# Kernel tuning notes

Hardware: AMD Instinct MI355X
Metric: run time of the kernel (lower is better)

Reference implementation:

```python
import jax, jax.numpy as jnp
import numpy as np

H, DK = 16, 64
F = H * DK  # n_feat = 1024
B, T = 2, 2048


def setup_inputs() -> dict:
    key = jax.random.key(0)
    ks = jax.random.split(key, 11)
    mk = lambda k, sh: jax.random.normal(k, sh, dtype=jnp.float32)
    inp = {
        "query": mk(ks[0], (B, T, F)),
        "key": mk(ks[1], (B, T, F)),
        "value": mk(ks[2], (B, T, F)),
    }
    # Standard RoPE frequency table, shaped [T,1,1,DK] to broadcast over [t,b,h,d].
    pos = jnp.arange(T, dtype=jnp.float32)[:, None]
    inv_freq = 1.0 / (10000.0 ** (jnp.arange(0, DK, 2, dtype=jnp.float32) / DK))
    ang = pos * inv_freq                       # [T, DK/2]
    emb = jnp.concatenate([ang, ang], axis=-1)  # [T, DK]
    inp["cos"] = jnp.cos(emb)[:, None, None, :]
    inp["sin"] = jnp.sin(emb)[:, None, None, :]
    scale = 1.0 / np.sqrt(F).astype(np.float32)
    for i, n in enumerate(["wq", "wk", "wv", "wo"]):
        inp[n] = mk(ks[3 + i], (F, F)) * scale  # torch Linear weight layout [out,in]
    for i, n in enumerate(["bq", "bk", "bv", "bo"]):
        inp[n] = mk(ks[7 + i], (F,)) * 0.01
    return inp


def _rtt_half(x):
    d = x.shape[-1]
    return jnp.concatenate([-x[..., d // 2:], x[..., :d // 2]], axis=-1)


def reference(query, key, value, cos, sin, wq, bq, wk, bk, wv, bv, wo, bo):
    b, t, f = query.shape
    h, d = H, DK
    # [b,t,f] -> [t,b,h,d] as in the torch code (RoPE applied pre-projection)
    to_tbhd = lambda x: jnp.swapaxes(x, 0, 1).reshape(t, b, h, d)
    q = to_tbhd(query)
    k = to_tbhd(key)
    c, s = cos[:t], sin[:t]
    q = q * c + _rtt_half(q) * s
    k = k * c + _rtt_half(k) * s
    back = lambda x: jnp.swapaxes(x.reshape(t, b, f), 0, 1)  # -> [b,t,f]
    q, k = back(q), back(k)
    lin = lambda x, w, bias: x @ w.T + bias
    Q = lin(q, wq, bq).reshape(b, t, h, d)
    K = lin(k, wk, bk).reshape(b, t, h, d)
    V = lin(value, wv, bv).reshape(b, t, h, d)
    scores = jnp.einsum('bqhd,bkhd->bhqk', Q, K) / jnp.sqrt(jnp.float32(d))
    attn = jax.nn.softmax(scores, axis=-1)
    o = jnp.einsum('bhqk,bkhd->bqhd', attn, V).reshape(b, t, f)
    return o @ wo.T + bo
```

## Files before the change

kernel.cpp:

```cpp
#include <hip/hip_runtime.h>
#include <hip/hip_bf16.h>

#define DEVI __device__ __forceinline__

typedef unsigned short u16;
typedef unsigned int u32;
typedef __attribute__((ext_vector_type(8))) short bf16x8;
typedef __attribute__((ext_vector_type(4))) short bf16x4;
typedef __attribute__((ext_vector_type(4))) float f32x4;

#define Bn 2
#define Tn 2048
#define Hn 16
#define Dn 64
#define Fn 1024

DEVI u16 tobf(float f) {
    __hip_bfloat16 h = __float2bfloat16(f);
    return __builtin_bit_cast(u16, h);
}
DEVI float frombf(u16 u) {
    return __builtin_bit_cast(float, ((u32)u) << 16);
}

DEVI f32x4 mfma16(bf16x8 a, bf16x8 b, f32x4 c) {
    return __builtin_amdgcn_mfma_f32_16x16x32_bf16(a, b, c, 0, 0, 0);
}

DEVI void gload_lds16(const u16* g, u16* l) {
    __builtin_amdgcn_global_load_lds(
        (const __attribute__((address_space(1))) void*)g,
        (__attribute__((address_space(3))) void*)l, 16, 0, 0);
}

__global__ __launch_bounds__(256) void k_prep(const float* __restrict__ q,
                                              const float* __restrict__ k,
                                              const float* __restrict__ v,
                                              const float* __restrict__ cosb,
                                              const float* __restrict__ sinb,
                                              const float* __restrict__ wq,
                                              const float* __restrict__ wk,
                                              const float* __restrict__ wv,
                                              const float* __restrict__ wo,
                                              u16* __restrict__ Aq,
                                              u16* __restrict__ Ak,
                                              u16* __restrict__ Av) {
    if (blockIdx.x < 4096) {
        unsigned idx = blockIdx.x * 256 + threadIdx.x;
        unsigned which = idx >> 19;
        unsigned r = idx & 0x7FFFFu;
        unsigned d0 = (r & 7u) << 2;
        unsigned h = (r >> 3) & 15u;
        unsigned t = (r >> 7) & 2047u;
        unsigned b = (r >> 18) & 1u;
        const float* src = which ? k : q;
        u16* dst = which ? Ak : Aq;
        size_t base = ((size_t)(b * Tn + t)) * Fn + h * Dn;
        float4 lo = *(const float4*)(src + base + d0);
        float4 hi = *(const float4*)(src + base + d0 + 32);
        float4 cl = *(const float4*)(cosb + (size_t)t * Dn + d0);
        float4 ch = *(const float4*)(cosb + (size_t)t * Dn + d0 + 32);
        float4 sl = *(const float4*)(sinb + (size_t)t * Dn + d0);
        float4 sh = *(const float4*)(sinb + (size_t)t * Dn + d0 + 32);
        bf16x4 olo, ohi;
        olo[0] = (short)tobf(lo.x * cl.x - hi.x * sl.x);
        olo[1] = (short)tobf(lo.y * cl.y - hi.y * sl.y);
        olo[2] = (short)tobf(lo.z * cl.z - hi.z * sl.z);
        olo[3] = (short)tobf(lo.w * cl.w - hi.w * sl.w);
        ohi[0] = (short)tobf(hi.x * ch.x + lo.x * sh.x);
        ohi[1] = (short)tobf(hi.y * ch.y + lo.y * sh.y);
        ohi[2] = (short)tobf(hi.z * ch.z + lo.z * sh.z);
        ohi[3] = (short)tobf(hi.w * ch.w + lo.w * sh.w);
        *(bf16x4*)(dst + base + d0) = olo;
        *(bf16x4*)(dst + base + d0 + 32) = ohi;
    } else {
        size_t i8 = (((size_t)blockIdx.x - 4096) * 256 + threadIdx.x) * 8;
        const size_t M4 = (size_t)4 << 20, M1 = (size_t)1 << 20;
        const float* src;
        size_t off;
        if (i8 < M4)              { src = v;  off = i8; }
        else if (i8 < M4 + M1)    { src = wq; off = i8 - M4; }
        else if (i8 < M4 + 2*M1)  { src = wk; off = i8 - M4 - M1; }
        else if (i8 < M4 + 3*M1)  { src = wv; off = i8 - M4 - 2*M1; }
        else                      { src = wo; off = i8 - M4 - 3*M1; }
        float4 a = *(const float4*)(src + off);
        float4 c = *(const float4*)(src + off + 4);
        bf16x8 vv;
        vv[0] = (short)tobf(a.x); vv[1] = (short)tobf(a.y);
        vv[2] = (short)tobf(a.z); vv[3] = (short)tobf(a.w);
        vv[4] = (short)tobf(c.x); vv[5] = (short)tobf(c.y);
        vv[6] = (short)tobf(c.z); vv[7] = (short)tobf(c.w);
        *(bf16x8*)(Av + i8) = vv;
    }
}

DEVI void store_out(u16* p, float v) { *p = tobf(v); }
DEVI void store_out(float* p, float v) { *p = v; }

template <typename OUT>
DEVI void gemm_body(const u16* __restrict__ A, const u16* __restrict__ W,
                    const float* __restrict__ bias, OUT* __restrict__ C,
                    float scale, u16* As, u16* Bs, int mode) {
    const int tid = threadIdx.x;
    const int lane = tid & 63;
    const int wave = tid >> 6;
    const int l15 = lane & 15, l4 = lane >> 4;
    const int bm = blockIdx.y << 7, bn = blockIdx.x << 7;
    const int wr = (wave >> 1) << 6, wc = (wave & 1) << 6;

    const int c0 = tid, c1 = tid + 256;
    const u16* A0p = A + (size_t)(bm + (c0 >> 2)) * 1024 + ((c0 & 3) << 3);
    const u16* A1p = A + (size_t)(bm + (c1 >> 2)) * 1024 + ((c1 & 3) << 3);
    const u16* B0p = W + (size_t)(bn + (c0 >> 2)) * 1024 + ((c0 & 3) << 3);
    const u16* B1p = W + (size_t)(bn + (c1 >> 2)) * 1024 + ((c1 & 3) << 3);
    u16* Ad0 = As + (c0 << 3);
    u16* Ad1 = As + (c1 << 3);
    u16* Bd0 = Bs + (c0 << 3);
    u16* Bd1 = Bs + (c1 << 3);

    f32x4 acc[4][4] = {};

    for (int k0 = 0; k0 < 1024; k0 += 32) {
        gload_lds16(A0p + k0, Ad0);
        gload_lds16(A1p + k0, Ad1);
        gload_lds16(B0p + k0, Bd0);
        gload_lds16(B1p + k0, Bd1);
        __syncthreads();
        bf16x8 af[4], bfr[4];
        #pragma unroll
        for (int m = 0; m < 4; m++)
            af[m] = *(const bf16x8*)(As + (wr + m * 16 + l15) * 32 + (l4 << 3));
        #pragma unroll
        for (int n = 0; n < 4; n++)
            bfr[n] = *(const bf16x8*)(Bs + (wc + n * 16 + l15) * 32 + (l4 << 3));
        #pragma unroll
        for (int m = 0; m < 4; m++)
            #pragma unroll
            for (int n = 0; n < 4; n++)
                acc[m][n] = mfma16(af[m], bfr[n], acc[m][n]);
        __syncthreads();
    }

    #pragma unroll
    for (int m = 0; m < 4; m++)
        #pragma unroll
        for (int n = 0; n < 4; n++) {
            const int gcol = bn + wc + n * 16 + l15;
            const float bb = bias[gcol];
            #pragma unroll
            for (int j = 0; j < 4; j++) {
                const int grow = bm + wr + m * 16 + (l4 << 2) + j;
                const float val = (acc[m][n][j] + bb) * scale;
                if (mode == 0) {
                    store_out(C + (size_t)grow * 1024 + gcol, val);
                } else {
                    const int b = grow >> 11, t = grow & 2047;
                    const int h = gcol >> 6, d = gcol & 63;
                    const int bh = b * 16 + h, tt2 = t >> 6, r = t & 63;
                    const size_t tbase = ((size_t)(bh * 32 + tt2)) << 12;
                    size_t off;
                    if (mode == 1) {
                        const int nn = ((r >> 5) << 1) | ((r >> 2) & 1);
                        const int kk = d >> 5, ll4 = (d >> 3) & 3, e = d & 7;
                        const int ll15 = (((r >> 3) & 3) << 2) | (r & 3);
                        off = tbase + ((size_t)(nn * 2 + kk) << 9) +
                              ((ll4 * 16 + ll15) << 3) + e;
                    } else {
                        const int kk = r >> 5, ll4 = (r >> 3) & 3, e = r & 7;
                        const int nd = d >> 4, ll15 = d & 15;
                        off = tbase + ((size_t)(kk * 4 + nd) << 9) +
                              ((ll4 * 16 + ll15) << 3) + e;
                    }
                    ((u16*)C)[off] = tobf(val);
                }
            }
        }
}

__global__ __launch_bounds__(256) void k_gemm_qkv(
    const u16* A0, const u16* W0, const float* b0, u16* C0,
    const u16* A1, const u16* W1, const float* b1, u16* C1,
    const u16* A2, const u16* W2, const float* b2, u16* C2) {
    __shared__ __align__(16) u16 As[128 * 32];
    __shared__ __align__(16) u16 Bs[128 * 32];
    const int z = blockIdx.z;
    const u16* A = z == 0 ? A0 : (z == 1 ? A1 : A2);
    const u16* W = z == 0 ? W0 : (z == 1 ? W1 : W2);
    const float* bias = z == 0 ? b0 : (z == 1 ? b1 : b2);
    u16* C = z == 0 ? C0 : (z == 1 ? C1 : C2);
    const float scale = z == 0 ? 0.125f * 1.4426950408889634f : 1.0f;
    gemm_body<u16>(A, W, bias, C, scale, As, Bs, z);
}

__global__ __launch_bounds__(256) void k_gemm_f32(const u16* __restrict__ A,
                                                  const u16* __restrict__ W,
                                                  const float* __restrict__ bias,
                                                  float* __restrict__ C) {
    __shared__ __align__(16) u16 As[128 * 32];
    __shared__ __align__(16) u16 Bs[128 * 32];
    gemm_body<float>(A, W, bias, C, 1.0f, As, Bs, 0);
}

__global__ __launch_bounds__(256) void k_attn(const u16* __restrict__ Qp,
                                              const u16* __restrict__ Kr,
                                              const u16* __restrict__ Vr,
                                              u16* __restrict__ Op0,
                                              u16* __restrict__ Op1,
                                              u16* __restrict__ Op2,
                                              u16* __restrict__ Op3,
                                              float* __restrict__ Ls) {
    const int tid = threadIdx.x, wave = tid >> 6, lane = tid & 63;
    const int l15 = lane & 15, l4 = lane >> 4;
    const int bh = blockIdx.x, b = bh >> 4, h = bh & 15;
    const int sp = blockIdx.z;
    const int q0 = blockIdx.y * 128 + wave * 32;
    const int tbase = sp << 3;

    bf16x8 aq[2][2];
    #pragma unroll
    for (int mq = 0; mq < 2; mq++)
        #pragma unroll
        for (int kk = 0; kk < 2; kk++)
            aq[mq][kk] = *(const bf16x8*)(Qp +
                ((size_t)(b * Tn + q0 + mq * 16 + l15)) * Fn + h * Dn + kk * 32 + (l4 << 3));

    f32x4 o[2][4] = {};
    float lrun[2] = {0.f, 0.f};
    const f32x4 zero4 = {0.f, 0.f, 0.f, 0.f};

    bf16x8 ones;
    #pragma unroll
    for (int j = 0; j < 8; j++) ones[j] = (short)0x3F80;

    const u16* Kbr = Kr + ((size_t)bh << 17);
    const u16* Vbr = Vr + ((size_t)bh << 17);
    const int lo8 = lane * 8;

    bf16x8 ka[4][2];
    #pragma unroll
    for (int n = 0; n < 4; n++)
        #pragma unroll
        for (int kk = 0; kk < 2; kk++)
            ka[n][kk] = *(const bf16x8*)(Kbr + ((tbase * 8 + n * 2 + kk) << 9) + lo8);

    #pragma unroll 1
    for (int tt = 0; tt < 8; tt++) {
        const int tg = tbase + tt;
        const int tn = (tt < 7) ? tg + 1 : tbase;
        bf16x8 va[2][4];
        #pragma unroll
        for (int kk = 0; kk < 2; kk++)
            #pragma unroll
            for (int nd = 0; nd < 4; nd++)
                va[kk][nd] = *(const bf16x8*)(Vbr + ((tg * 8 + kk * 4 + nd) << 9) + lo8);

        f32x4 s[2][4];
        __builtin_amdgcn_s_setprio(1);
        #pragma unroll
        for (int n = 0; n < 4; n++) {
            s[0][n] = mfma16(ka[n][0], aq[0][0], zero4);
            s[1][n] = mfma16(ka[n][0], aq[1][0], zero4);
            s[0][n] = mfma16(ka[n][1], aq[0][1], s[0][n]);
            s[1][n] = mfma16(ka[n][1], aq[1][1], s[1][n]);
        }
        __builtin_amdgcn_s_setprio(0);

        #pragma unroll
        for (int n = 0; n < 4; n++)
            #pragma unroll
            for (int kk = 0; kk < 2; kk++)
                ka[n][kk] = *(const bf16x8*)(Kbr + ((tn * 8 + n * 2 + kk) << 9) + lo8);

        bf16x8 pb[2][2];
        #pragma unroll
        for (int mq = 0; mq < 2; mq++)
            #pragma unroll
            for (int kk = 0; kk < 2; kk++) {
                float p0 = __builtin_amdgcn_exp2f(s[mq][2 * kk][0]);
                float p1 = __builtin_amdgcn_exp2f(s[mq][2 * kk][1]);
                float p2 = __builtin_amdgcn_exp2f(s[mq][2 * kk][2]);
                float p3 = __builtin_amdgcn_exp2f(s[mq][2 * kk][3]);
                float p4 = __builtin_amdgcn_exp2f(s[mq][2 * kk + 1][0]);
                float p5 = __builtin_amdgcn_exp2f(s[mq][2 * kk + 1][1]);
                float p6 = __builtin_amdgcn_exp2f(s[mq][2 * kk + 1][2]);
                float p7 = __builtin_amdgcn_exp2f(s[mq][2 * kk + 1][3]);
                bf16x8 pv;
                pv[0] = (short)tobf(p0); pv[1] = (short)tobf(p1);
                pv[2] = (short)tobf(p2); pv[3] = (short)tobf(p3);
                pv[4] = (short)tobf(p4); pv[5] = (short)tobf(p5);
                pv[6] = (short)tobf(p6); pv[7] = (short)tobf(p7);
                pb[mq][kk] = pv;
            }

        __builtin_amdgcn_s_setprio(1);
        f32x4 osum0 = mfma16(ones, pb[0][0], zero4);
        f32x4 osum1 = mfma16(ones, pb[1][0], zero4);
        osum0 = mfma16(ones, pb[0][1], osum0);
        osum1 = mfma16(ones, pb[1][1], osum1);
        #pragma unroll
        for (int kk = 0; kk < 2; kk++)
            #pragma unroll
            for (int nd = 0; nd < 4; nd++) {
                o[0][nd] = mfma16(va[kk][nd], pb[0][kk], o[0][nd]);
                o[1][nd] = mfma16(va[kk][nd], pb[1][kk], o[1][nd]);
            }
        __builtin_amdgcn_s_setprio(0);
        lrun[0] += osum0[0];
        lrun[1] += osum1[0];
    }

    u16* OpS = sp == 0 ? Op0 : (sp == 1 ? Op1 : (sp == 2 ? Op2 : Op3));
    #pragma unroll
    for (int mq = 0; mq < 2; mq++) {
        const int q = q0 + mq * 16 + l15;
        float inv = 1.f / lrun[mq];
        #pragma unroll
        for (int nd = 0; nd < 4; nd++) {
            bf16x4 ov;
            ov[0] = (short)tobf(o[mq][nd][0] * inv);
            ov[1] = (short)tobf(o[mq][nd][1] * inv);
            ov[2] = (short)tobf(o[mq][nd][2] * inv);
            ov[3] = (short)tobf(o[mq][nd][3] * inv);
            *(bf16x4*)(OpS + ((size_t)(b * Tn + q)) * Fn +
                       h * Dn + nd * 16 + (l4 << 2)) = ov;
        }
        if (l4 == 0)
            Ls[(((size_t)(sp * 2 + b)) * Tn + q) * Hn + h] = lrun[mq];
    }
}

__global__ __launch_bounds__(256) void k_combine(const u16* __restrict__ Op0,
                                                 const u16* __restrict__ Op1,
                                                 const u16* __restrict__ Op2,
                                                 const u16* __restrict__ Op3,
                                                 const float* __restrict__ Ls,
                                                 u16* __restrict__ Oa) {
    size_t e0 = ((size_t)blockIdx.x * 256 + threadIdx.x) * 8;
    int row = (int)(e0 >> 10);
    int b = row >> 11, q = row & 2047;
    int h = (int)(e0 >> 6) & 15;
    float l0 = Ls[(((size_t)(0 + b)) * Tn + q) * Hn + h];
    float l1 = Ls[(((size_t)(2 + b)) * Tn + q) * Hn + h];
    float l2 = Ls[(((size_t)(4 + b)) * Tn + q) * Hn + h];
    float l3 = Ls[(((size_t)(6 + b)) * Tn + q) * Hn + h];
    float inv = 1.f / (l0 + l1 + l2 + l3);
    float w0 = l0 * inv, w1 = l1 * inv, w2 = l2 * inv, w3 = l3 * inv;
    bf16x8 x0 = *(const bf16x8*)(Op0 + e0);
    bf16x8 x1 = *(const bf16x8*)(Op1 + e0);
    bf16x8 x2 = *(const bf16x8*)(Op2 + e0);
    bf16x8 x3 = *(const bf16x8*)(Op3 + e0);
    bf16x8 out;
    #pragma unroll
    for (int j = 0; j < 8; j++)
        out[j] = (short)tobf(frombf((u16)x0[j]) * w0 + frombf((u16)x1[j]) * w1 +
                             frombf((u16)x2[j]) * w2 + frombf((u16)x3[j]) * w3);
    *(bf16x8*)(Oa + e0) = out;
}

extern "C" void kernel_launch(void* const* d_in, const int* in_sizes, int n_in,
                              void* d_out, int out_size, void* d_ws, size_t ws_size,
                              hipStream_t stream) {
    const float* q    = (const float*)d_in[0];
    const float* k    = (const float*)d_in[1];
    const float* v    = (const float*)d_in[2];
    const float* cosb = (const float*)d_in[3];
    const float* sinb = (const float*)d_in[4];
    const float* wq   = (const float*)d_in[5];
    const float* wk   = (const float*)d_in[6];
    const float* wv   = (const float*)d_in[7];
    const float* wo   = (const float*)d_in[8];
    const float* bq   = (const float*)d_in[9];
    const float* bk   = (const float*)d_in[10];
    const float* bv   = (const float*)d_in[11];
    const float* bo   = (const float*)d_in[12];

    char* ws = (char*)d_ws;
    char* dob = (char*)d_out;
    const size_t MB = (size_t)1 << 20;
    u16* Aq  = (u16*)(ws);
    u16* Ak  = (u16*)(ws + 8 * MB);
    u16* Av  = (u16*)(ws + 16 * MB);
    u16* Wq  = (u16*)(ws + 24 * MB);
    u16* Wk  = (u16*)(ws + 26 * MB);
    u16* Wv  = (u16*)(ws + 28 * MB);
    u16* Wo  = (u16*)(ws + 30 * MB);
    u16* Qp  = (u16*)(ws + 32 * MB);
    u16* Kr  = (u16*)(ws + 40 * MB);
    u16* Vr  = (u16*)(ws + 48 * MB);
    u16* Op0 = (u16*)(dob);
    u16* Op1 = (u16*)(dob + 8 * MB);
    u16* Op2 = (u16*)(ws);
    u16* Op3 = (u16*)(ws + 8 * MB);
    float* Ls = (float*)(ws + 16 * MB);
    u16* Oa  = (u16*)(ws);

    k_prep<<<8192, 256, 0, stream>>>(q, k, v, cosb, sinb, wq, wk, wv, wo,
                                     Aq, Ak, Av);
    k_gemm_qkv<<<dim3(8, 32, 3), 256, 0, stream>>>(Aq, Wq, bq, Qp,
                                                   Ak, Wk, bk, Kr,
                                                   Av, Wv, bv, Vr);
    k_attn<<<dim3(32, 16, 4), 256, 0, stream>>>(Qp, Kr, Vr, Op0, Op1, Op2, Op3, Ls);
    k_combine<<<2048, 256, 0, stream>>>(Op0, Op1, Op2, Op3, Ls, Oa);
    k_gemm_f32<<<dim3(8, 32), 256, 0, stream>>>(Oa, Wo, bo, (float*)d_out);
}
```

Before: 146.4 us.

## Stage K/V tiles through double-buffered LDS with direct global-to-LDS loads

Each wave previously loaded the full K and V tiles from global memory into registers on its own. Now the four waves cooperatively load each K/V tile once into double-buffered shared memory using direct global-to-LDS copies, prefetching the next tile while the current one is computed. This cuts redundant global/L2 traffic by sharing tiles across waves. In exchange it adds a block-wide barrier per iteration and LDS reads, and may lower occupancy because of the extra shared memory.

```diff
diff --git a/kernel.cpp b/kernel.cpp
--- a/kernel.cpp
+++ b/kernel.cpp
@@ -209,6 +209,8 @@
                                               u16* __restrict__ Op2,
                                               u16* __restrict__ Op3,
                                               float* __restrict__ Ls) {
+    __shared__ __align__(16) u16 Ks[2][4096];
+    __shared__ __align__(16) u16 Vs[2][4096];
     const int tid = threadIdx.x, wave = tid >> 6, lane = tid & 63;
     const int l15 = lane & 15, l4 = lane >> 4;
     const int bh = blockIdx.x, b = bh >> 4, h = bh & 15;
@@ -236,23 +238,35 @@
     const u16* Vbr = Vr + ((size_t)bh << 17);
     const int lo8 = lane * 8;
 
-    bf16x8 ka[4][2];
-    #pragma unroll
-    for (int n = 0; n < 4; n++)
-        #pragma unroll
-        for (int kk = 0; kk < 2; kk++)
-            ka[n][kk] = *(const bf16x8*)(Kbr + ((tbase * 8 + n * 2 + kk) << 9) + lo8);
+    #define STAGE(bf, tg)                                                     \
+        _Pragma("unroll")                                                     \
+        for (int i = 0; i < 2; i++) {                                         \
+            const int c = wave + i * 4;                                       \
+            gload_lds16(Kbr + (((tg) * 8 + c) << 9) + lo8,                    \
+                        &Ks[bf][(c << 9) + lo8]);                             \
+            gload_lds16(Vbr + (((tg) * 8 + c) << 9) + lo8,                    \
+                        &Vs[bf][(c << 9) + lo8]);                             \
+        }
+
+    STAGE(0, tbase);
+    __syncthreads();
+    int cur = 0;
 
     #pragma unroll 1
     for (int tt = 0; tt < 8; tt++) {
-        const int tg = tbase + tt;
-        const int tn = (tt < 7) ? tg + 1 : tbase;
-        bf16x8 va[2][4];
+        if (tt < 7) STAGE(cur ^ 1, tbase + tt + 1);
+
+        bf16x8 ka[4][2], va[2][4];
+        #pragma unroll
+        for (int n = 0; n < 4; n++)
+            #pragma unroll
+            for (int kk = 0; kk < 2; kk++)
+                ka[n][kk] = *(const bf16x8*)(&Ks[cur][((n * 2 + kk) << 9) + lo8]);
         #pragma unroll
         for (int kk = 0; kk < 2; kk++)
             #pragma unroll
             for (int nd = 0; nd < 4; nd++)
-                va[kk][nd] = *(const bf16x8*)(Vbr + ((tg * 8 + kk * 4 + nd) << 9) + lo8);
+                va[kk][nd] = *(const bf16x8*)(&Vs[cur][((kk * 4 + nd) << 9) + lo8]);
 
         f32x4 s[2][4];
         __builtin_amdgcn_s_setprio(1);
@@ -264,12 +278,6 @@
             s[1][n] = mfma16(ka[n][1], aq[1][1], s[1][n]);
         }
         __builtin_amdgcn_s_setprio(0);
-
-        #pragma unroll
-        for (int n = 0; n < 4; n++)
-            #pragma unroll
-            for (int kk = 0; kk < 2; kk++)
-                ka[n][kk] = *(const bf16x8*)(Kbr + ((tn * 8 + n * 2 + kk) << 9) + lo8);
 
         bf16x8 pb[2][2];
         #pragma unroll
@@ -307,7 +315,11 @@
         __builtin_amdgcn_s_setprio(0);
         lrun[0] += osum0[0];
         lrun[1] += osum1[0];
+
+        __syncthreads();
+        cur ^= 1;
     }
+    #undef STAGE
 
     u16* OpS = sp == 0 ? Op0 : (sp == 1 ? Op1 : (sp == 2 ? Op2 : Op3));
     #pragma unroll
```

Measured after the change: 139.3 us. 1.05x faster.
